# Kernel optimization log

Hardware: AMD Instinct MI355X
Metric: run time of the kernel (lower is better)

Reference implementation:

```python
import jax, jax.numpy as jnp
import numpy as np
from jax import lax

BS, CNT, W, P, E, K, L = 32, 128, 2048, 1024, 8, 25, 2


def setup_inputs() -> dict:
    key = jax.random.key(0)
    ks = jax.random.split(key, 12)
    s = lambda k, shape, scale: jax.random.normal(k, shape, dtype=jnp.float32) * scale
    return {
        "x": s(ks[0], (BS, CNT, W), 1.0),
        "conv_w": s(ks[1], (L, E, 1, K), 0.2),
        "conv_b": s(ks[2], (L, E), 0.02),
        "wq": s(ks[3], (L, P, W), 0.02),
        "bq": s(ks[4], (L, P), 0.02),
        "wk": s(ks[5], (L, P, W), 0.02),
        "bk": s(ks[6], (L, P), 0.02),
        "wv": s(ks[7], (L, P, W), 0.02),
        "bv": s(ks[8], (L, P), 0.02),
        "wo": s(ks[9], (L, W, P), 0.02),
        "bo": s(ks[10], (L, W), 0.02),
    }


def _moe(x, w, b):
    # x: [bs, cnt, W]; w: [E, 1, K]; b: [E]
    bs, cnt, d = x.shape
    xf = x.reshape(bs * cnt, 1, d)
    pad = K // 2
    y = lax.conv_general_dilated(
        xf, w, window_strides=(1,), padding=[(pad, pad)],
        dimension_numbers=("NCH", "OIH", "NCH"))  # [bs*cnt, E, W]
    y = y + b[None, :, None]
    return y.mean(axis=1).reshape(bs, cnt, d)


def _fe(x, wq, bq, wk, bk, wv, bv, wo, bo):
    # x: [bs, cnt, W]; projections to P, FFT-domain attention, back to W
    q = jnp.einsum("bcw,pw->bcp", x, wq) + bq
    k = jnp.einsum("bcw,pw->bcp", x, wk) + bk
    v = jnp.einsum("bcw,pw->bcp", x, wv) + bv
    q_fft = jnp.fft.fft(q, axis=-1)
    k_fft = jnp.fft.fft(k, axis=-1)
    v_fft = jnp.fft.fft(v, axis=-1)
    scale = jnp.sqrt(jnp.float32(P))
    weighted = (k_fft * jnp.conj(q_fft)) / scale * v_fft
    wv_real = jnp.fft.ifft(weighted, axis=-1).real.astype(x.dtype)
    return jnp.einsum("bcp,wp->bcw", wv_real, wo) + bo


def reference(x, conv_w, conv_b, wq, bq, wk, bk, wv, bv, wo, bo):
    for l in range(L):
        x = _moe(x, conv_w[l], conv_b[l])
        x = _fe(x, wq[l], bq[l], wk[l], bk[l], wv[l], bv[l], wo[l], bo[l])
    return x
```

## Files before the change

### kernel.cpp

```cpp
#include <hip/hip_runtime.h>
#include <hip/hip_bf16.h>

#define BSZ 32
#define CNTS 128
#define WD 2048
#define PD 1024
#define ED 8
#define KSZ 25
#define LN 2
#define MROWS (BSZ*CNTS)
#define QKVN (3*PD)
#define NWL (PD*WD)

typedef _Float16 f16;
typedef __attribute__((ext_vector_type(8))) _Float16 f16x8;
typedef __attribute__((ext_vector_type(4))) float f32x4;
typedef __attribute__((ext_vector_type(2))) float f32x2;

#define PI_F 3.14159265358979323846f
#define PAD(a) ((a) + ((a) >> 5))

__global__ __launch_bounds__(256) void cvt_layer(
    const float* __restrict__ wq, const float* __restrict__ wk,
    const float* __restrict__ wv, const float* __restrict__ wo,
    f16* __restrict__ wqkv16, f16* __restrict__ wo16)
{
    const int i = (blockIdx.x * 256 + threadIdx.x) * 4;
    const float* src;
    f16* dst;
    if (i < 3*NWL) {
        dst = wqkv16 + i;
        src = (i < NWL) ? wq + i : (i < 2*NWL) ? wk + (i - NWL) : wv + (i - 2*NWL);
    } else {
        dst = wo16 + (i - 3*NWL);
        src = wo + (i - 3*NWL);
    }
    const float4 v = *(const float4*)src;
    f16 o[4];
    o[0] = (f16)v.x; o[1] = (f16)v.y; o[2] = (f16)v.z; o[3] = (f16)v.w;
    *(ushort4*)dst = *(const ushort4*)o;
}

template<typename IT>
__global__ __launch_bounds__(256) void conv_moe(
    const IT* __restrict__ xin,
    const float* __restrict__ cw,
    const float* __restrict__ cb,
    f16* __restrict__ xo)
{
    __shared__ float srow[WD];
    __shared__ float swb[KSZ];
    __shared__ float sbb;
    const int tid = threadIdx.x;
    const size_t row = blockIdx.x;
    if (tid < KSZ) {
        float s = 0.f;
        for (int e = 0; e < ED; ++e) s += cw[e*KSZ + tid];
        swb[tid] = s * (1.f/ED);
    }
    if (tid == 32) {
        float s = 0.f;
        for (int e = 0; e < ED; ++e) s += cb[e];
        sbb = s * (1.f/ED);
    }
    const IT* xr = xin + row*WD;
    for (int i = tid; i < WD; i += 256) srow[i] = (float)xr[i];
    __syncthreads();
    const float bb = sbb;
    for (int t0 = 0; t0 < WD; t0 += 256) {
        const int t = t0 + tid;
        float acc = bb;
        #pragma unroll
        for (int k = 0; k < KSZ; ++k) {
            const int idx = t + k - (KSZ/2);
            const float xv = (idx >= 0 && idx < WD) ? srow[idx] : 0.f;
            acc = fmaf(xv, swb[k], acc);
        }
        xo[row*WD + t] = (f16)acc;
    }
}

template<typename OT>
__global__ __launch_bounds__(256, 2) void gemm_f16(
    const f16* __restrict__ A,
    const f16* __restrict__ B,
    const float* __restrict__ c0, const float* __restrict__ c1, const float* __restrict__ c2,
    OT* __restrict__ out,
    const int K, const int N)
{
    __shared__ f16 sA[128*64];
    __shared__ f16 sB[128*64];
    const int tid  = threadIdx.x;
    const int m0   = blockIdx.x * 128;
    const int n0   = blockIdx.y * 128;
    const int lane = tid & 63;
    const int wave = tid >> 6;
    const int wm   = (wave >> 1) * 64;
    const int wn   = (wave & 1) * 64;
    const int quad = lane >> 4;
    const int r16  = lane & 15;

    f32x4 acc[4][4] = {};

    int aoff[4];
    #pragma unroll
    for (int t = 0; t < 4; ++t) {
        const int s = tid + 256*t;
        const int row = s >> 3;
        const int sc8 = ((s & 7) ^ (row & 7)) * 8;
        aoff[t] = row * K + sc8;
    }

    int aBase[4], aXor[4], bBase[4], bXor[4];
    #pragma unroll
    for (int i = 0; i < 4; ++i) {
        const int ra = wm + i*16 + r16;
        aBase[i] = ra << 3; aXor[i] = ra & 7;
        const int rb = wn + i*16 + r16;
        bBase[i] = rb << 3; bXor[i] = rb & 7;
    }

    const size_t mK = (size_t)m0 * K;
    const size_t nK = (size_t)n0 * K;

    for (int kb = 0; kb < K; kb += 64) {
        #pragma unroll
        for (int t = 0; t < 4; ++t) {
            const int s = tid + 256*t;
            __builtin_amdgcn_global_load_lds(
                (const __attribute__((address_space(1))) unsigned int*)(A + mK + aoff[t] + kb),
                (__attribute__((address_space(3))) unsigned int*)&sA[s*8], 16, 0, 0);
            __builtin_amdgcn_global_load_lds(
                (const __attribute__((address_space(1))) unsigned int*)(B + nK + aoff[t] + kb),
                (__attribute__((address_space(3))) unsigned int*)&sB[s*8], 16, 0, 0);
        }
        __syncthreads();

        #pragma unroll
        for (int ks = 0; ks < 2; ++ks) {
            const int c = ks*4 + quad;
            f16x8 af[4], bfm[4];
            #pragma unroll
            for (int i = 0; i < 4; ++i)
                af[i] = *(const f16x8*)&sA[(aBase[i] | (c ^ aXor[i])) * 8];
            #pragma unroll
            for (int j = 0; j < 4; ++j)
                bfm[j] = *(const f16x8*)&sB[(bBase[j] | (c ^ bXor[j])) * 8];
            #pragma unroll
            for (int i = 0; i < 4; ++i)
                #pragma unroll
                for (int j = 0; j < 4; ++j)
                    acc[i][j] = __builtin_amdgcn_mfma_f32_16x16x32_f16(af[i], bfm[j], acc[i][j], 0, 0, 0);
        }
        __syncthreads();
    }

    #pragma unroll
    for (int j = 0; j < 4; ++j) {
        const int col = n0 + wn + j*16 + r16;
        const float bv = (col < 1024) ? c0[col] : (col < 2048) ? c1[col-1024] : c2[col-2048];
        #pragma unroll
        for (int i = 0; i < 4; ++i) {
            #pragma unroll
            for (int r = 0; r < 4; ++r) {
                const int rowg = m0 + wm + i*16 + quad*4 + r;
                out[(size_t)rowg*N + col] = (OT)(acc[i][j][r] + bv);
            }
        }
    }
}

__global__ __launch_bounds__(512, 2) void gemm192(
    const f16* __restrict__ A,
    const f16* __restrict__ B,
    const float* __restrict__ c0, const float* __restrict__ c1, const float* __restrict__ c2,
    f16* __restrict__ out,
    const int K, const int N)
{
    __shared__ __align__(16) f16 sA[2][2][128*64];
    __shared__ __align__(16) f16 sB[2][3][64*64];

    const int tid  = threadIdx.x;
    const int lane = tid & 63;
    const int wave = tid >> 6;
    const int wr   = wave >> 2;
    const int wc   = wave & 3;
    const int quad = lane >> 4;
    const int r16  = lane & 15;
    const int xrA  = r16 & 7;

    const int orig = blockIdx.x;
    const int xcd  = orig & 7;
    const int loc  = orig >> 3;
    const int mt   = (xcd >> 1) * 4 + (loc & 3);
    const int nt   = (xcd & 1) * 8 + (loc >> 2);
    const int m0   = mt * 256;
    const int n0   = nt * 192;

    f32x4 acc[8][3] = {};
    f16x8 bf[3][2];
    f16x8 aX0, aX1, aX2, aX3, aY0, aY1, aY2, aY3, aZ0, aZ1, aZ2, aZ3;

    int soffA[2];
    #pragma unroll
    for (int t = 0; t < 2; ++t) {
        const int s = tid + 512*t;
        const int row = s >> 3;
        soffA[t] = row * K + (((s & 7) ^ (row & 7)) * 8);
    }
    int soffB;
    {
        const int row = tid >> 3;
        soffB = row * K + (((tid & 7) ^ (row & 7)) * 8);
    }

    int bPiece[3], bBase[3], bXor[3];
    #pragma unroll
    for (int j = 0; j < 3; ++j) {
        const int rb = wc*48 + j*16 + r16;
        bPiece[j] = rb >> 6;
        bBase[j]  = (rb & 63) << 3;
        bXor[j]   = rb & 7;
    }

    const f16* Abase[2] = { A + (size_t)m0 * K, A + (size_t)(m0 + 128) * K };
    const f16* Bp[3]    = { B + (size_t)n0 * K, B + (size_t)(n0 + 64) * K,
                            B + (size_t)(n0 + 128) * K };

    #define STAGE_A(BUF, HALF, GOFF)                                              \
      { _Pragma("unroll") for (int t = 0; t < 2; ++t) {                           \
          __builtin_amdgcn_global_load_lds(                                       \
            (const __attribute__((address_space(1))) unsigned int*)(Abase[HALF] + soffA[t] + (GOFF)), \
            (__attribute__((address_space(3))) unsigned int*)&sA[BUF][HALF][(tid + 512*t)*8], \
            16, 0, 0); } }

    #define STAGE_B(BUF, PIECE, GOFF)                                             \
      { __builtin_amdgcn_global_load_lds(                                         \
          (const __attribute__((address_space(1))) unsigned int*)(Bp[PIECE] + soffB + (GOFF)), \
          (__attribute__((address_space(3))) unsigned int*)&sB[BUF][PIECE][tid*8], \
          16, 0, 0); }

    #define LDA(BUF, ROW, C) \
      (*(const f16x8*)&sA[BUF][wr][ (((ROW) << 3) + ((C) ^ xrA)) * 8 ])

    #define LDB(BUF, J, C) \
      (*(const f16x8*)&sB[BUF][bPiece[J]][ (bBase[J] + ((C) ^ bXor[J])) * 8 ])

    #define READ_BF(BUF)                                                          \
      { _Pragma("unroll") for (int j = 0; j < 3; ++j) {                           \
          bf[j][0] = LDB(BUF, j, quad);                                           \
          bf[j][1] = LDB(BUF, j, 4 + quad);                                       \
        } }

    #define READ_A(BUF, Q, D0, D1, D2, D3)                                        \
      D0 = LDA(BUF, (2*(Q))*16   + r16, quad);                                    \
      D1 = LDA(BUF, (2*(Q))*16   + r16, 4 + quad);                                \
      D2 = LDA(BUF, (2*(Q)+1)*16 + r16, quad);                                    \
      D3 = LDA(BUF, (2*(Q)+1)*16 + r16, 4 + quad);

    #define MFMA_Q(Q, D0, D1, D2, D3)                                             \
      __builtin_amdgcn_s_setprio(1);                                              \
      { _Pragma("unroll") for (int jj = 0; jj < 3; ++jj) {                        \
          acc[2*(Q)][jj]   = __builtin_amdgcn_mfma_f32_16x16x32_f16(D0, bf[jj][0], acc[2*(Q)][jj],   0,0,0); \
          acc[2*(Q)+1][jj] = __builtin_amdgcn_mfma_f32_16x16x32_f16(D2, bf[jj][0], acc[2*(Q)+1][jj], 0,0,0); \
        } }                                                                       \
      { _Pragma("unroll") for (int jj = 0; jj < 3; ++jj) {                        \
          acc[2*(Q)][jj]   = __builtin_amdgcn_mfma_f32_16x16x32_f16(D1, bf[jj][1], acc[2*(Q)][jj],   0,0,0); \
          acc[2*(Q)+1][jj] = __builtin_amdgcn_mfma_f32_16x16x32_f16(D3, bf[jj][1], acc[2*(Q)+1][jj], 0,0,0); \
        } }                                                                       \
      __builtin_amdgcn_s_setprio(0);

    #define LGKM(n) asm volatile("s_waitcnt lgkmcnt(" #n ")" ::: "memory");       \
                    __builtin_amdgcn_sched_barrier(0);
    #define VMC(n)  asm volatile("s_waitcnt vmcnt(" #n ")" ::: "memory");
    #define BAR()   __builtin_amdgcn_s_barrier();

    STAGE_B(0, 0, 0); STAGE_B(0, 1, 0); STAGE_B(0, 2, 0);
    STAGE_A(0, 0, 0); STAGE_A(0, 1, 0);
    STAGE_B(1, 0, 64); STAGE_B(1, 1, 64); STAGE_B(1, 2, 64);
    VMC(3)
    BAR()

    const int NIT = K >> 7;
    for (int it = 0; it < NIT; ++it) {
        const bool kl = (it == NIT - 1);
        const int kb1 = (2*it + 1) * 64;
        const int kb2 = kb1 + 64;
        const int kb3 = kb1 + 128;

        STAGE_A(1, 0, kb1);
        READ_BF(0)
        READ_A(0, 0, aX0, aX1, aX2, aX3)
        LGKM(0)
        MFMA_Q(0, aX0, aX1, aX2, aX3)
        BAR()
        STAGE_A(1, 1, kb1);
        READ_A(0, 1, aY0, aY1, aY2, aY3)
        READ_A(0, 2, aZ0, aZ1, aZ2, aZ3)
        LGKM(4)
        MFMA_Q(1, aY0, aY1, aY2, aY3)
        if (!kl) { STAGE_B(0, 0, kb2); STAGE_B(0, 1, kb2); }
        READ_A(0, 3, aX0, aX1, aX2, aX3)
        LGKM(4)
        MFMA_Q(2, aZ0, aZ1, aZ2, aZ3)
        if (!kl) { STAGE_B(0, 2, kb2); }
        LGKM(0)
        MFMA_Q(3, aX0, aX1, aX2, aX3)
        if (!kl) { VMC(3) } else { VMC(0) }
        BAR()

        if (!kl) STAGE_A(0, 0, kb2);
        READ_BF(1)
        READ_A(1, 0, aX0, aX1, aX2, aX3)
        LGKM(0)
        MFMA_Q(0, aX0, aX1, aX2, aX3)
        BAR()
        if (!kl) STAGE_A(0, 1, kb2);
        READ_A(1, 1, aY0, aY1, aY2, aY3)
        READ_A(1, 2, aZ0, aZ1, aZ2, aZ3)
        LGKM(4)
        MFMA_Q(1, aY0, aY1, aY2, aY3)
        if (!kl) { STAGE_B(1, 0, kb3); STAGE_B(1, 1, kb3); }
        READ_A(1, 3, aX0, aX1, aX2, aX3)
        LGKM(4)
        MFMA_Q(2, aZ0, aZ1, aZ2, aZ3)
        if (!kl) { STAGE_B(1, 2, kb3); }
        LGKM(0)
        MFMA_Q(3, aX0, aX1, aX2, aX3)
        if (!kl) { VMC(3) }
        BAR()
    }

    #pragma unroll
    for (int j = 0; j < 3; ++j) {
        const int col = n0 + wc*48 + j*16 + r16;
        const float bv = (col < 1024) ? c0[col] : (col < 2048) ? c1[col-1024] : c2[col-2048];
        #pragma unroll
        for (int mi = 0; mi < 8; ++mi) {
            #pragma unroll
            for (int r = 0; r < 4; ++r) {
                const int rowg = m0 + wr*128 + mi*16 + quad*4 + r;
                out[(size_t)rowg*N + col] = (f16)(acc[mi][j][r] + bv);
            }
        }
    }

    #undef STAGE_A
    #undef STAGE_B
    #undef LDA
    #undef LDB
    #undef READ_BF
    #undef READ_A
    #undef MFMA_Q
    #undef LGKM
    #undef VMC
    #undef BAR
}

__device__ inline void fft1024r4(f32x2* x, f32x2* y, const int tid)
{
    f32x2* src = x;
    f32x2* dst = y;
    #pragma unroll
    for (int st = 0; st < 5; ++st) {
        const int ls = 2*st;
        const int s  = 1 << ls;
        const int p  = tid >> ls;
        const int q  = tid & (s - 1);
        const float invn = 1.f / (float)(1024 >> ls);
        const f32x2 a = src[PAD(tid)];
        const f32x2 b = src[PAD(tid + 256)];
        const f32x2 c = src[PAD(tid + 512)];
        const f32x2 d = src[PAD(tid + 768)];
        float ws, wc;
        __sincosf(-2.f*PI_F * (float)p * invn, &ws, &wc);
        const float apcx = a.x + c.x, apcy = a.y + c.y;
        const float amcx = a.x - c.x, amcy = a.y - c.y;
        const float bpdx = b.x + d.x, bpdy = b.y + d.y;
        const float bmdx = b.x - d.x, bmdy = b.y - d.y;
        f32x2 y0; y0.x = apcx + bpdx; y0.y = apcy + bpdy;
        const float t1x = amcx + bmdy, t1y = amcy - bmdx;
        const float t2x = apcx - bpdx, t2y = apcy - bpdy;
        const float t3x = amcx - bmdy, t3y = amcy + bmdx;
        const float w2x = wc*wc - ws*ws, w2y = 2.f*wc*ws;
        const float w3x = w2x*wc - w2y*ws, w3y = w2x*ws + w2y*wc;
        f32x2 y1; y1.x = wc*t1x - ws*t1y;   y1.y = wc*t1y + ws*t1x;
        f32x2 y2; y2.x = w2x*t2x - w2y*t2y; y2.y = w2x*t2y + w2y*t2x;
        f32x2 y3; y3.x = w3x*t3x - w3y*t3y; y3.y = w3x*t3y + w3y*t3x;
        const int base = q + ((p * s) << 2);
        dst[PAD(base)]       = y0;
        dst[PAD(base + s)]   = y1;
        dst[PAD(base + 2*s)] = y2;
        dst[PAD(base + 3*s)] = y3;
        __syncthreads();
        f32x2* t = src; src = dst; dst = t;
    }
}

__global__ __launch_bounds__(256) void fft_attn2(
    const f16* __restrict__ qkv, f16* __restrict__ outg)
{
    __shared__ f32x2 X[PAD(1023)+1], Y[PAD(1023)+1];
    const int tid = threadIdx.x;
    const size_t row0 = (size_t)blockIdx.x * 2;
    const f16* r1 = qkv + row0*QKVN;
    const f16* r2 = r1 + QKVN;

    f32x2 V1[4], V2[4], S1[4], S2[4];

    #pragma unroll
    for (int k = 0; k < 4; ++k) {
        const int i = tid + 256*k;
        f32x2 t; t.x = (float)r1[2048+i]; t.y = (float)r2[2048+i];
        X[PAD(i)] = t;
    }
    __syncthreads();
    fft1024r4(X, Y, tid);
    #pragma unroll
    for (int k = 0; k < 4; ++k) {
        const int f = tid + 256*k;
        const int g = (PD - f) & (PD-1);
        const f32x2 z1 = Y[PAD(f)], z2 = Y[PAD(g)];
        V1[k].x = 0.5f*(z1.x + z2.x); V1[k].y = 0.5f*(z1.y - z2.y);
        V2[k].x = 0.5f*(z1.y + z2.y); V2[k].y = 0.5f*(z2.x - z1.x);
    }

    #pragma unroll
    for (int k = 0; k < 4; ++k) {
        const int i = tid + 256*k;
        f32x2 t; t.x = (float)r1[i]; t.y = (float)r1[1024+i];
        X[PAD(i)] = t;
    }
    __syncthreads();
    fft1024r4(X, Y, tid);
    #pragma unroll
    for (int k = 0; k < 4; ++k) {
        const int f = tid + 256*k;
        const int g = (PD - f) & (PD-1);
        const f32x2 z1 = Y[PAD(f)], z2 = Y[PAD(g)];
        const float Qr = 0.5f*(z1.x + z2.x), Qi = 0.5f*(z1.y - z2.y);
        const float Kr = 0.5f*(z1.y + z2.y), Ki = 0.5f*(z2.x - z1.x);
        const float Pr = (Kr*Qr + Ki*Qi) * (1.f/32.f);
        const float Pi = (Ki*Qr - Kr*Qi) * (1.f/32.f);
        S1[k].x = Pr*V1[k].x - Pi*V1[k].y;
        S1[k].y = -(Pr*V1[k].y + Pi*V1[k].x);
    }

    #pragma unroll
    for (int k = 0; k < 4; ++k) {
        const int i = tid + 256*k;
        f32x2 t; t.x = (float)r2[i]; t.y = (float)r2[1024+i];
        X[PAD(i)] = t;
    }
    __syncthreads();
    fft1024r4(X, Y, tid);
    #pragma unroll
    for (int k = 0; k < 4; ++k) {
        const int f = tid + 256*k;
        const int g = (PD - f) & (PD-1);
        const f32x2 z1 = Y[PAD(f)], z2 = Y[PAD(g)];
        const float Qr = 0.5f*(z1.x + z2.x), Qi = 0.5f*(z1.y - z2.y);
        const float Kr = 0.5f*(z1.y + z2.y), Ki = 0.5f*(z2.x - z1.x);
        const float Pr = (Kr*Qr + Ki*Qi) * (1.f/32.f);
        const float Pi = (Ki*Qr - Kr*Qi) * (1.f/32.f);
        S2[k].x = Pr*V2[k].x - Pi*V2[k].y;
        S2[k].y = -(Pr*V2[k].y + Pi*V2[k].x);
    }

    #pragma unroll
    for (int k = 0; k < 4; ++k) {
        const int f = tid + 256*k;
        f32x2 t; t.x = S1[k].x - S2[k].y; t.y = S1[k].y + S2[k].x;
        X[PAD(f)] = t;
    }
    __syncthreads();
    fft1024r4(X, Y, tid);
    f16* o1 = outg + row0*PD;
    f16* o2 = o1 + PD;
    #pragma unroll
    for (int k = 0; k < 4; ++k) {
        const int n = tid + 256*k;
        const f32x2 z = Y[PAD(n)];
        o1[n] = (f16)(z.x * (1.f/1024.f));
        o2[n] = (f16)(z.y * (1.f/1024.f));
    }
}

extern "C" void kernel_launch(void* const* d_in, const int* in_sizes, int n_in,
                              void* d_out, int out_size, void* d_ws, size_t ws_size,
                              hipStream_t stream)
{
    const float* x      = (const float*)d_in[0];
    const float* conv_w = (const float*)d_in[1];
    const float* conv_b = (const float*)d_in[2];
    const float* wq     = (const float*)d_in[3];
    const float* bq     = (const float*)d_in[4];
    const float* wk     = (const float*)d_in[5];
    const float* bk     = (const float*)d_in[6];
    const float* wv     = (const float*)d_in[7];
    const float* bv     = (const float*)d_in[8];
    const float* wo     = (const float*)d_in[9];
    const float* bo     = (const float*)d_in[10];

    char* ws = (char*)d_ws;
    const size_t MB = 1024*1024;
    f16*   wqkv16 = (f16*)(ws);
    f16*   wo16   = (f16*)(ws + 12*MB);
    f16*   qkvbuf = (f16*)(ws + 16*MB);
    f16*   xc16   = (f16*)(ws + 40*MB);
    f16*   xmid   = (f16*)(ws + 56*MB);
    f16*   wvr16  = xc16;

    for (int l = 0; l < LN; ++l) {
        cvt_layer<<<dim3(4*NWL/4/256), dim3(256), 0, stream>>>(
            wq + (size_t)l*NWL, wk + (size_t)l*NWL, wv + (size_t)l*NWL, wo + (size_t)l*NWL,
            wqkv16, wo16);

        if (l == 0)
            conv_moe<float><<<dim3(MROWS), dim3(256), 0, stream>>>(
                x, conv_w, conv_b, xc16);
        else
            conv_moe<f16><<<dim3(MROWS), dim3(256), 0, stream>>>(
                xmid, conv_w + (size_t)l*ED*KSZ, conv_b + (size_t)l*ED, xc16);

        gemm192<<<dim3((MROWS/256)*(QKVN/192)), dim3(512), 0, stream>>>(
            xc16, wqkv16,
            bq + (size_t)l*PD, bk + (size_t)l*PD, bv + (size_t)l*PD,
            qkvbuf, WD, QKVN);

        fft_attn2<<<dim3(MROWS/2), dim3(256), 0, stream>>>(qkvbuf, wvr16);

        if (l == LN-1)
            gemm_f16<float><<<dim3(MROWS/128, WD/128), dim3(256), 0, stream>>>(
                wvr16, wo16,
                bo + (size_t)l*WD, bo + (size_t)l*WD + PD, bo + (size_t)l*WD + PD,
                (float*)d_out, PD, WD);
        else
            gemm_f16<f16><<<dim3(MROWS/128, WD/128), dim3(256), 0, stream>>>(
                wvr16, wo16,
                bo + (size_t)l*WD, bo + (size_t)l*WD + PD, bo + (size_t)l*WD + PD,
                xmid, PD, WD);
    }
}
```

Measured before the change: 402.5 us.

## Restructure QKV GEMM to 128x192 tiles with triple-buffered LDS and staged stores

Replaces the 256x192 double-buffered QKV GEMM with a 128x192 tile kernel that uses a three-deep LDS ring, loading each 64-wide K slice two steps ahead with one barrier per step. The grid doubles to 512 blocks, which is meant to improve CU coverage and cut the hand-interleaved schedule down to a simpler load-then-MFMA loop. The epilogue now writes results through an LDS bounce buffer so global stores are 16-byte vectorised rows instead of scattered 2-byte writes. The cost is lower arithmetic intensity per block and less overlap of LDS reads with MFMA inside a step.

```diff
diff --git a/kernel.cpp b/kernel.cpp
--- a/kernel.cpp
+++ b/kernel.cpp
@@ -170,15 +170,15 @@
     }
 }
 
-__global__ __launch_bounds__(512, 2) void gemm192(
+__global__ __launch_bounds__(512, 1) void gemmQKV(
     const f16* __restrict__ A,
     const f16* __restrict__ B,
     const float* __restrict__ c0, const float* __restrict__ c1, const float* __restrict__ c2,
     f16* __restrict__ out,
     const int K, const int N)
 {
-    __shared__ __align__(16) f16 sA[2][2][128*64];
-    __shared__ __align__(16) f16 sB[2][3][64*64];
+    __shared__ __align__(16) f16 sA[3][128*64];
+    __shared__ __align__(16) f16 sB[3][192*64];
 
     const int tid  = threadIdx.x;
     const int lane = tid & 63;
@@ -187,19 +187,16 @@
     const int wc   = wave & 3;
     const int quad = lane >> 4;
     const int r16  = lane & 15;
-    const int xrA  = r16 & 7;
 
     const int orig = blockIdx.x;
     const int xcd  = orig & 7;
     const int loc  = orig >> 3;
-    const int mt   = (xcd >> 1) * 4 + (loc & 3);
-    const int nt   = (xcd & 1) * 8 + (loc >> 2);
-    const int m0   = mt * 256;
+    const int mt   = (xcd >> 1) * 8 + (loc & 7);
+    const int nt   = (xcd & 1) * 8 + (loc >> 3);
+    const int m0   = mt * 128;
     const int n0   = nt * 192;
 
-    f32x4 acc[8][3] = {};
-    f16x8 bf[3][2];
-    f16x8 aX0, aX1, aX2, aX3, aY0, aY1, aY2, aY3, aZ0, aZ1, aZ2, aZ3;
+    f32x4 acc[4][3] = {};
 
     int soffA[2];
     #pragma unroll
@@ -208,151 +205,119 @@
         const int row = s >> 3;
         soffA[t] = row * K + (((s & 7) ^ (row & 7)) * 8);
     }
-    int soffB;
-    {
-        const int row = tid >> 3;
-        soffB = row * K + (((tid & 7) ^ (row & 7)) * 8);
-    }
-
-    int bPiece[3], bBase[3], bXor[3];
-    #pragma unroll
-    for (int j = 0; j < 3; ++j) {
-        const int rb = wc*48 + j*16 + r16;
-        bPiece[j] = rb >> 6;
-        bBase[j]  = (rb & 63) << 3;
-        bXor[j]   = rb & 7;
-    }
-
-    const f16* Abase[2] = { A + (size_t)m0 * K, A + (size_t)(m0 + 128) * K };
-    const f16* Bp[3]    = { B + (size_t)n0 * K, B + (size_t)(n0 + 64) * K,
-                            B + (size_t)(n0 + 128) * K };
-
-    #define STAGE_A(BUF, HALF, GOFF)                                              \
+    int soffB[3];
+    #pragma unroll
+    for (int t = 0; t < 3; ++t) {
+        const int s = tid + 512*t;
+        const int row = s >> 3;
+        soffB[t] = row * K + (((s & 7) ^ (row & 7)) * 8);
+    }
+
+    const f16* Ab = A + (size_t)m0 * K;
+    const f16* Bb = B + (size_t)n0 * K;
+
+    #define STAGE_A(BUF, GOFF)                                                    \
       { _Pragma("unroll") for (int t = 0; t < 2; ++t) {                           \
           __builtin_amdgcn_global_load_lds(                                       \
-            (const __attribute__((address_space(1))) unsigned int*)(Abase[HALF] + soffA[t] + (GOFF)), \
-            (__attribute__((address_space(3))) unsigned int*)&sA[BUF][HALF][(tid + 512*t)*8], \
+            (const __attribute__((address_space(1))) unsigned int*)(Ab + soffA[t] + (GOFF)), \
+            (__attribute__((address_space(3))) unsigned int*)&sA[BUF][(tid + 512*t)*8], \
             16, 0, 0); } }
 
-    #define STAGE_B(BUF, PIECE, GOFF)                                             \
-      { __builtin_amdgcn_global_load_lds(                                         \
-          (const __attribute__((address_space(1))) unsigned int*)(Bp[PIECE] + soffB + (GOFF)), \
-          (__attribute__((address_space(3))) unsigned int*)&sB[BUF][PIECE][tid*8], \
-          16, 0, 0); }
+    #define STAGE_B(BUF, GOFF)                                                    \
+      { _Pragma("unroll") for (int t = 0; t < 3; ++t) {                           \
+          __builtin_amdgcn_global_load_lds(                                       \
+            (const __attribute__((address_space(1))) unsigned int*)(Bb + soffB[t] + (GOFF)), \
+            (__attribute__((address_space(3))) unsigned int*)&sB[BUF][(tid + 512*t)*8], \
+            16, 0, 0); } }
 
     #define LDA(BUF, ROW, C) \
-      (*(const f16x8*)&sA[BUF][wr][ (((ROW) << 3) + ((C) ^ xrA)) * 8 ])
-
-    #define LDB(BUF, J, C) \
-      (*(const f16x8*)&sB[BUF][bPiece[J]][ (bBase[J] + ((C) ^ bXor[J])) * 8 ])
-
-    #define READ_BF(BUF)                                                          \
-      { _Pragma("unroll") for (int j = 0; j < 3; ++j) {                           \
-          bf[j][0] = LDB(BUF, j, quad);                                           \
-          bf[j][1] = LDB(BUF, j, 4 + quad);                                       \
-        } }
-
-    #define READ_A(BUF, Q, D0, D1, D2, D3)                                        \
-      D0 = LDA(BUF, (2*(Q))*16   + r16, quad);                                    \
-      D1 = LDA(BUF, (2*(Q))*16   + r16, 4 + quad);                                \
-      D2 = LDA(BUF, (2*(Q)+1)*16 + r16, quad);                                    \
-      D3 = LDA(BUF, (2*(Q)+1)*16 + r16, 4 + quad);
-
-    #define MFMA_Q(Q, D0, D1, D2, D3)                                             \
-      __builtin_amdgcn_s_setprio(1);                                              \
-      { _Pragma("unroll") for (int jj = 0; jj < 3; ++jj) {                        \
-          acc[2*(Q)][jj]   = __builtin_amdgcn_mfma_f32_16x16x32_f16(D0, bf[jj][0], acc[2*(Q)][jj],   0,0,0); \
-          acc[2*(Q)+1][jj] = __builtin_amdgcn_mfma_f32_16x16x32_f16(D2, bf[jj][0], acc[2*(Q)+1][jj], 0,0,0); \
-        } }                                                                       \
-      { _Pragma("unroll") for (int jj = 0; jj < 3; ++jj) {                        \
-          acc[2*(Q)][jj]   = __builtin_amdgcn_mfma_f32_16x16x32_f16(D1, bf[jj][1], acc[2*(Q)][jj],   0,0,0); \
-          acc[2*(Q)+1][jj] = __builtin_amdgcn_mfma_f32_16x16x32_f16(D3, bf[jj][1], acc[2*(Q)+1][jj], 0,0,0); \
-        } }                                                                       \
-      __builtin_amdgcn_s_setprio(0);
-
-    #define LGKM(n) asm volatile("s_waitcnt lgkmcnt(" #n ")" ::: "memory");       \
-                    __builtin_amdgcn_sched_barrier(0);
+      (*(const f16x8*)&sA[BUF][ (((ROW) << 3) | ((C) ^ ((ROW) & 7))) * 8 ])
+    #define LDB(BUF, ROW, C) \
+      (*(const f16x8*)&sB[BUF][ (((ROW) << 3) | ((C) ^ ((ROW) & 7))) * 8 ])
+
     #define VMC(n)  asm volatile("s_waitcnt vmcnt(" #n ")" ::: "memory");
     #define BAR()   __builtin_amdgcn_s_barrier();
 
-    STAGE_B(0, 0, 0); STAGE_B(0, 1, 0); STAGE_B(0, 2, 0);
-    STAGE_A(0, 0, 0); STAGE_A(0, 1, 0);
-    STAGE_B(1, 0, 64); STAGE_B(1, 1, 64); STAGE_B(1, 2, 64);
-    VMC(3)
+    STAGE_A(0, 0); STAGE_B(0, 0);
+    STAGE_A(1, 64); STAGE_B(1, 64);
+    VMC(5)
     BAR()
 
-    const int NIT = K >> 7;
-    for (int it = 0; it < NIT; ++it) {
-        const bool kl = (it == NIT - 1);
-        const int kb1 = (2*it + 1) * 64;
-        const int kb2 = kb1 + 64;
-        const int kb3 = kb1 + 128;
-
-        STAGE_A(1, 0, kb1);
-        READ_BF(0)
-        READ_A(0, 0, aX0, aX1, aX2, aX3)
-        LGKM(0)
-        MFMA_Q(0, aX0, aX1, aX2, aX3)
+    const int NT = K >> 6;
+    int cur = 0;
+    for (int t = 0; t < NT; ++t) {
+        const int nx2 = (cur >= 1) ? cur - 1 : cur + 2;
+
+        if (t < NT-2) {
+            const int kb2 = (t + 2) << 6;
+            STAGE_A(nx2, kb2);
+            STAGE_B(nx2, kb2);
+        }
+
+        f16x8 af[4][2], bfr[3][2];
+        #pragma unroll
+        for (int mi = 0; mi < 4; ++mi) {
+            const int ra = wr*64 + mi*16 + r16;
+            af[mi][0] = LDA(cur, ra, quad);
+            af[mi][1] = LDA(cur, ra, 4 + quad);
+        }
+        #pragma unroll
+        for (int j = 0; j < 3; ++j) {
+            const int rb = wc*48 + j*16 + r16;
+            bfr[j][0] = LDB(cur, rb, quad);
+            bfr[j][1] = LDB(cur, rb, 4 + quad);
+        }
+        asm volatile("s_waitcnt lgkmcnt(0)" ::: "memory");
+        __builtin_amdgcn_sched_barrier(0);
+
+        __builtin_amdgcn_s_setprio(1);
+        #pragma unroll
+        for (int mi = 0; mi < 4; ++mi)
+            #pragma unroll
+            for (int j = 0; j < 3; ++j)
+                acc[mi][j] = __builtin_amdgcn_mfma_f32_16x16x32_f16(af[mi][0], bfr[j][0], acc[mi][j], 0, 0, 0);
+        #pragma unroll
+        for (int mi = 0; mi < 4; ++mi)
+            #pragma unroll
+            for (int j = 0; j < 3; ++j)
+                acc[mi][j] = __builtin_amdgcn_mfma_f32_16x16x32_f16(af[mi][1], bfr[j][1], acc[mi][j], 0, 0, 0);
+        __builtin_amdgcn_s_setprio(0);
+
+        if (t < NT-2) { VMC(5) } else { VMC(0) }
         BAR()
-        STAGE_A(1, 1, kb1);
-        READ_A(0, 1, aY0, aY1, aY2, aY3)
-        READ_A(0, 2, aZ0, aZ1, aZ2, aZ3)
-        LGKM(4)
-        MFMA_Q(1, aY0, aY1, aY2, aY3)
-        if (!kl) { STAGE_B(0, 0, kb2); STAGE_B(0, 1, kb2); }
-        READ_A(0, 3, aX0, aX1, aX2, aX3)
-        LGKM(4)
-        MFMA_Q(2, aZ0, aZ1, aZ2, aZ3)
-        if (!kl) { STAGE_B(0, 2, kb2); }
-        LGKM(0)
-        MFMA_Q(3, aX0, aX1, aX2, aX3)
-        if (!kl) { VMC(3) } else { VMC(0) }
-        BAR()
-
-        if (!kl) STAGE_A(0, 0, kb2);
-        READ_BF(1)
-        READ_A(1, 0, aX0, aX1, aX2, aX3)
-        LGKM(0)
-        MFMA_Q(0, aX0, aX1, aX2, aX3)
-        BAR()
-        if (!kl) STAGE_A(0, 1, kb2);
-        READ_A(1, 1, aY0, aY1, aY2, aY3)
-        READ_A(1, 2, aZ0, aZ1, aZ2, aZ3)
-        LGKM(4)
-        MFMA_Q(1, aY0, aY1, aY2, aY3)
-        if (!kl) { STAGE_B(1, 0, kb3); STAGE_B(1, 1, kb3); }
-        READ_A(1, 3, aX0, aX1, aX2, aX3)
-        LGKM(4)
-        MFMA_Q(2, aZ0, aZ1, aZ2, aZ3)
-        if (!kl) { STAGE_B(1, 2, kb3); }
-        LGKM(0)
-        MFMA_Q(3, aX0, aX1, aX2, aX3)
-        if (!kl) { VMC(3) }
-        BAR()
-    }
-
+
+        cur = (cur == 2) ? 0 : cur + 1;
+    }
+
+    f16* bounce = (f16*)&sB[0][0];
     #pragma unroll
     for (int j = 0; j < 3; ++j) {
-        const int col = n0 + wc*48 + j*16 + r16;
+        const int colt = wc*48 + j*16 + r16;
+        const int col  = n0 + colt;
         const float bv = (col < 1024) ? c0[col] : (col < 2048) ? c1[col-1024] : c2[col-2048];
         #pragma unroll
-        for (int mi = 0; mi < 8; ++mi) {
+        for (int mi = 0; mi < 4; ++mi) {
             #pragma unroll
             for (int r = 0; r < 4; ++r) {
-                const int rowg = m0 + wr*128 + mi*16 + quad*4 + r;
-                out[(size_t)rowg*N + col] = (f16)(acc[mi][j][r] + bv);
+                const int rowt = wr*64 + mi*16 + quad*4 + r;
+                bounce[rowt*200 + colt] = (f16)(acc[mi][j][r] + bv);
             }
         }
+    }
+    BAR()
+    #pragma unroll
+    for (int p = 0; p < 6; ++p) {
+        const int g   = tid + 512*p;
+        const int row = g / 24;
+        const int k   = g - row*24;
+        const f16x8 v = *(const f16x8*)&bounce[row*200 + k*8];
+        *(f16x8*)&out[(size_t)(m0 + row)*N + n0 + k*8] = v;
     }
 
     #undef STAGE_A
     #undef STAGE_B
     #undef LDA
     #undef LDB
-    #undef READ_BF
-    #undef READ_A
-    #undef MFMA_Q
-    #undef LGKM
     #undef VMC
     #undef BAR
 }
@@ -523,7 +488,7 @@
             conv_moe<f16><<<dim3(MROWS), dim3(256), 0, stream>>>(
                 xmid, conv_w + (size_t)l*ED*KSZ, conv_b + (size_t)l*ED, xc16);
 
-        gemm192<<<dim3((MROWS/256)*(QKVN/192)), dim3(512), 0, stream>>>(
+        gemmQKV<<<dim3((MROWS/128)*(QKVN/192)), dim3(512), 0, stream>>>(
             xc16, wqkv16,
             bq + (size_t)l*PD, bk + (size_t)l*PD, bv + (size_t)l*PD,
             qkvbuf, WD, QKVN);
```

Result: slower. 443.8 us (+10.3%).
